# Kernel optimization log

Hardware: AMD Instinct MI355X
Metric: run time of the kernel (lower is better)

## Reference

```python
import jax, jax.numpy as jnp
import numpy as np

RANK = 4
ALPHA = 4.0
SCALE = ALPHA / RANK


def setup_inputs() -> dict:
    key = jax.random.key(0)
    k1, k2, k3, k4 = jax.random.split(key, 4)
    B, S, H = 4, 2048, 2048
    NH, HD = 16, 128
    x = jax.random.normal(k1, (B, S, H), dtype=jnp.float32)
    W_orig = jax.random.normal(k2, (H, NH, HD), dtype=jnp.float32) * (1.0 / np.sqrt(H))
    A_kernel = jax.random.normal(k3, (H, RANK), dtype=jnp.float32) * (1.0 / RANK)
    # B kernel is zero-init in the module; use small randn so the LoRA path is exercised
    B_kernel = jax.random.normal(k4, (RANK, NH, HD), dtype=jnp.float32) * 0.02
    return {"x": x, "W_orig": W_orig, "A_kernel": A_kernel, "B_kernel": B_kernel}


def reference(x, W_orig, A_kernel, B_kernel):
    # original layer: EinsumDense 'abc,cde->abde'  [B,S,H] x [H,NH,HD] -> [B,S,NH,HD]
    original_output = jnp.einsum('bsc,chd->bshd', x, W_orig)
    # LoRA path: Dense to rank, then EinsumDense back up, scaled
    ax = x @ A_kernel                                   # [B,S,r]
    lora_output = jnp.einsum('bsr,rhd->bshd', ax, B_kernel) * SCALE
    return original_output + lora_output
```

## Files before the change

### kernel.cpp

```cpp
#include <hip/hip_runtime.h>
#include <hip/hip_bf16.h>
#include <cstdint>


using bf16 = __hip_bfloat16;
typedef __attribute__((ext_vector_type(8))) __bf16 bf16x8;
typedef __attribute__((ext_vector_type(4))) float f32x4;

constexpr int Mdim = 8192;
constexpr int Ndim = 2048;
constexpr int Kdim = 2048;
constexpr float SCALE = 1.0f;

constexpr int BM = 256, BN = 256, BK = 64;
constexpr int NT2 = Kdim / (2 * BK);
constexpr int CVT_BLOCKS = (Mdim * Kdim) / (256 * 8);
constexpr int PREP_BLOCKS = (Ndim / 64) * (Kdim / 64);

__device__ __forceinline__ void gload_lds16(const void* g, void* l) {
  __builtin_amdgcn_global_load_lds(
      (const __attribute__((address_space(1))) uint32_t*)g,
      (__attribute__((address_space(3))) uint32_t*)l,
      16, 0, 0);
}

__global__ void prep_all(const float* __restrict__ X,
                         const float* __restrict__ W,
                         const float* __restrict__ A,
                         const float* __restrict__ Bk,
                         uint16_t* __restrict__ Xb,
                         uint16_t* __restrict__ Wt) {
  __shared__ float tile[64][65];

  if (blockIdx.x < CVT_BLOCKS) {
    const int i = blockIdx.x * blockDim.x + threadIdx.x;
    const float4* Xv = (const float4*)X;
    float4 a = Xv[i * 2 + 0];
    float4 b = Xv[i * 2 + 1];
    uint16_t o[8];
    o[0] = __bfloat16_as_ushort(__float2bfloat16(a.x));
    o[1] = __bfloat16_as_ushort(__float2bfloat16(a.y));
    o[2] = __bfloat16_as_ushort(__float2bfloat16(a.z));
    o[3] = __bfloat16_as_ushort(__float2bfloat16(a.w));
    o[4] = __bfloat16_as_ushort(__float2bfloat16(b.x));
    o[5] = __bfloat16_as_ushort(__float2bfloat16(b.y));
    o[6] = __bfloat16_as_ushort(__float2bfloat16(b.z));
    o[7] = __bfloat16_as_ushort(__float2bfloat16(b.w));
    *reinterpret_cast<uint4*>(Xb + (size_t)i * 8) = *reinterpret_cast<uint4*>(o);
  } else {
    const int pid = blockIdx.x - CVT_BLOCKS;
    const int tx = threadIdx.x & 63;
    const int ty = threadIdx.x >> 6;
    const int n0 = (pid & 31) * 64, k0 = (pid >> 5) * 64;

    const int n = n0 + tx;
    const float b0 = Bk[0 * Ndim + n];
    const float b1 = Bk[1 * Ndim + n];
    const float b2 = Bk[2 * Ndim + n];
    const float b3 = Bk[3 * Ndim + n];

    for (int i = ty; i < 64; i += 4) {
      const int k = k0 + i;
      float w = W[(size_t)k * Ndim + n];
      w += SCALE * (A[k * 4 + 0] * b0 + A[k * 4 + 1] * b1 +
                    A[k * 4 + 2] * b2 + A[k * 4 + 3] * b3);
      tile[tx][i] = w;
    }
    __syncthreads();
    for (int i = ty; i < 64; i += 4) {
      Wt[(size_t)(n0 + i) * Kdim + (k0 + tx)] =
          __bfloat16_as_ushort(__float2bfloat16(tile[i][tx]));
    }
  }
}

#define FENCE() asm volatile("" ::: "memory")
#define VMW(N)  asm volatile("s_waitcnt vmcnt(" #N ")" ::: "memory")
#define PMID()                                                                 \
  do {                                                                         \
    FENCE();                                                                   \
    __builtin_amdgcn_s_barrier();                                              \
    asm volatile("s_waitcnt lgkmcnt(0)" ::: "memory");                         \
  } while (0)
#define PEND()                                                                 \
  do {                                                                         \
    FENCE();                                                                   \
    __builtin_amdgcn_s_barrier();                                              \
    FENCE();                                                                   \
  } while (0)

__global__ __launch_bounds__(512, 2) void gemm_8ph(
    const uint16_t* __restrict__ X, const uint16_t* __restrict__ Wt,
    float* __restrict__ out) {
  __shared__ uint16_t lds[65536];

  const int t = threadIdx.x;
  const int wave = t >> 6, lane = t & 63;
  const int wm = wave >> 2, wn = wave & 3;
  const int l15 = lane & 15, kg = lane >> 4;
  const int sw = l15 & 7;

  const int lid = blockIdx.x;
  const int xcd = lid & 7, loc = lid >> 3;
  const int by = xcd * 4 + (loc & 3);
  const int bx = loc >> 2;
  const int m0 = by * BM, n0 = bx * BN;

  const uint16_t* Ag = X + (size_t)m0 * Kdim;
  const uint16_t* Bg = Wt + (size_t)n0 * Kdim;

  const int r8 = lane >> 3;
  const int gc = (lane & 7) ^ r8;
  const int slot0 = wave * 2, slot1 = slot0 + 1;
  const size_t go0 = (size_t)(slot0 * 8 + r8) * Kdim + gc * 8;
  const size_t go1 = (size_t)(slot1 * 8 + r8) * Kdim + gc * 8;

  int aE[2], bE[2];
#pragma unroll
  for (int s2 = 0; s2 < 2; ++s2) {
    const int p = (s2 * 4 + kg) ^ sw;
    aE[s2] = (wm * 64 + l15) * 64 + p * 8;
    bE[s2] = (wn * 32 + l15) * 64 + p * 8;
  }

#define STAGE_A(buf, h, kt)                                                    \
  do {                                                                         \
    gload_lds16(Ag + go0 + (size_t)(h) * 128 * Kdim + (kt),                    \
                &lds[(buf) * 32768 + (h) * 8192 + slot0 * 512]);               \
    gload_lds16(Ag + go1 + (size_t)(h) * 128 * Kdim + (kt),                    \
                &lds[(buf) * 32768 + (h) * 8192 + slot1 * 512]);               \
  } while (0)
#define STAGE_B(buf, h, kt)                                                    \
  do {                                                                         \
    gload_lds16(Bg + go0 + (size_t)(h) * 128 * Kdim + (kt),                    \
                &lds[(buf) * 32768 + 16384 + (h) * 8192 + slot0 * 512]);       \
    gload_lds16(Bg + go1 + (size_t)(h) * 128 * Kdim + (kt),                    \
                &lds[(buf) * 32768 + 16384 + (h) * 8192 + slot1 * 512]);       \
  } while (0)

  bf16x8 a[4][2], b[2][2];
  f32x4 acc[8][4] = {};

#define READ_A(QM, buf)                                                        \
  do {                                                                         \
    _Pragma("unroll") for (int ii = 0; ii < 4; ++ii)                           \
        _Pragma("unroll") for (int s2 = 0; s2 < 2; ++s2)                       \
            a[ii][s2] = *reinterpret_cast<const bf16x8*>(                      \
                &lds[(buf) * 32768 + (QM) * 8192 + ii * 1024 + aE[s2]]);       \
  } while (0)
#define READ_B(QN, buf)                                                        \
  do {                                                                         \
    _Pragma("unroll") for (int jj = 0; jj < 2; ++jj)                           \
        _Pragma("unroll") for (int s2 = 0; s2 < 2; ++s2)                       \
            b[jj][s2] = *reinterpret_cast<const bf16x8*>(                      \
                &lds[(buf) * 32768 + 16384 + (QN) * 8192 + jj * 1024 +         \
                     bE[s2]]);                                                 \
  } while (0)
#define MMA(QM, QN)                                                            \
  do {                                                                         \
    __builtin_amdgcn_s_setprio(1);                                             \
    _Pragma("unroll") for (int s2 = 0; s2 < 2; ++s2)                           \
        _Pragma("unroll") for (int ii = 0; ii < 4; ++ii)                       \
            _Pragma("unroll") for (int jj = 0; jj < 2; ++jj)                   \
                acc[(QM) * 4 + ii][(QN) * 2 + jj] =                            \
                    __builtin_amdgcn_mfma_f32_16x16x32_bf16(                   \
                        a[ii][s2], b[jj][s2],                                  \
                        acc[(QM) * 4 + ii][(QN) * 2 + jj], 0, 0, 0);           \
    __builtin_amdgcn_s_setprio(0);                                             \
  } while (0)

  STAGE_A(0, 0, 0); STAGE_B(0, 0, 0); STAGE_A(0, 1, 0); STAGE_B(0, 1, 0);
  FENCE();
  STAGE_A(1, 0, BK); STAGE_B(1, 0, BK); STAGE_A(1, 1, BK);
  FENCE();
  VMW(6);
  __builtin_amdgcn_s_barrier();
  FENCE();

#pragma unroll 1
  for (int j = 0; j < NT2; ++j) {
    const int kt1 = j * 128 + 64;
    const int kn0 = j * 128 + 128;
    const int kn1 = j * 128 + 192;
    const bool full = (j < NT2 - 1);

    STAGE_B(1, 1, kt1);
    VMW(8);
    READ_A(0, 0); READ_B(0, 0);
    PMID(); MMA(0, 0); PEND();

    if (full) STAGE_A(0, 0, kn0);
    READ_B(1, 0);
    PMID(); MMA(0, 1); PEND();

    READ_A(1, 0); READ_B(0, 0);
    PMID(); MMA(1, 0); PEND();

    if (full) { STAGE_B(0, 0, kn0); STAGE_A(0, 1, kn0); VMW(8); }
    else      { VMW(2); }
    READ_B(1, 0);
    PMID(); MMA(1, 1); PEND();

    if (full) { STAGE_B(0, 1, kn0); VMW(8); }
    else      { VMW(0); }
    READ_A(0, 1); READ_B(0, 1);
    PMID(); MMA(0, 0); PEND();

    if (full) STAGE_A(1, 0, kn1);
    READ_B(1, 1);
    PMID(); MMA(0, 1); PEND();

    READ_A(1, 1); READ_B(0, 1);
    PMID(); MMA(1, 0); PEND();

    if (full) { STAGE_B(1, 0, kn1); STAGE_A(1, 1, kn1); VMW(8); }
    READ_B(1, 1);
    PMID(); MMA(1, 1); PEND();
  }

#pragma unroll
  for (int i = 0; i < 8; ++i) {
    const int mb = m0 + (i >> 2) * 128 + wm * 64 + (i & 3) * 16 + kg * 4;
#pragma unroll
    for (int jn = 0; jn < 4; ++jn) {
      const int n = n0 + (jn >> 1) * 128 + wn * 32 + (jn & 1) * 16 + l15;
#pragma unroll
      for (int r = 0; r < 4; ++r) {
        out[(size_t)(mb + r) * Ndim + n] = acc[i][jn][r];
      }
    }
  }
#undef STAGE_A
#undef STAGE_B
#undef READ_A
#undef READ_B
#undef MMA
}

extern "C" void kernel_launch(void* const* d_in, const int* in_sizes, int n_in,
                              void* d_out, int out_size, void* d_ws, size_t ws_size,
                              hipStream_t stream) {
  const float* x  = (const float*)d_in[0];
  const float* W  = (const float*)d_in[1];
  const float* A  = (const float*)d_in[2];
  const float* Bk = (const float*)d_in[3];
  float* out = (float*)d_out;

  uint16_t* Xb = (uint16_t*)d_ws;
  uint16_t* Wt = (uint16_t*)((char*)d_ws + (size_t)Mdim * Kdim * 2);

  prep_all<<<CVT_BLOCKS + PREP_BLOCKS, 256, 0, stream>>>(x, W, A, Bk, Xb, Wt);

  gemm_8ph<<<(Mdim / BM) * (Ndim / BN), 512, 0, stream>>>(Xb, Wt, out);
}
```

Measured before the change: 197.2 us.

## Double-buffer B fragments in registers and reorder MMA phases to cut LDS reads

Keeps two B register fragments (b0, b1) so the phase order becomes (0,0),(0,1),(1,1),(1,0). This lets each B fragment be reused across two MMA phases, removing two of the four B re-reads from LDS per half-iteration. The global-to-LDS staging schedule and vmcnt waits are rearranged to match, and an early lgkmcnt(8) wait is added. The cost is more VGPR pressure at a 2-wave occupancy target, and the hand-tuned waitcnt counts could create hazards if they are wrong.

```diff
diff --git a/kernel.cpp b/kernel.cpp
--- a/kernel.cpp
+++ b/kernel.cpp
@@ -76,6 +76,7 @@
 
 #define FENCE() asm volatile("" ::: "memory")
 #define VMW(N)  asm volatile("s_waitcnt vmcnt(" #N ")" ::: "memory")
+#define LGKM8() asm volatile("s_waitcnt lgkmcnt(8)" ::: "memory")
 #define PMID()                                                                 \
   do {                                                                         \
     FENCE();                                                                   \
@@ -138,7 +139,7 @@
                 &lds[(buf) * 32768 + 16384 + (h) * 8192 + slot1 * 512]);       \
   } while (0)
 
-  bf16x8 a[4][2], b[2][2];
+  bf16x8 a[4][2], b0[2][2], b1[2][2];
   f32x4 acc[8][4] = {};
 
 #define READ_A(QM, buf)                                                        \
@@ -148,15 +149,15 @@
             a[ii][s2] = *reinterpret_cast<const bf16x8*>(                      \
                 &lds[(buf) * 32768 + (QM) * 8192 + ii * 1024 + aE[s2]]);       \
   } while (0)
-#define READ_B(QN, buf)                                                        \
+#define READ_B(QN, buf, dst)                                                   \
   do {                                                                         \
     _Pragma("unroll") for (int jj = 0; jj < 2; ++jj)                           \
         _Pragma("unroll") for (int s2 = 0; s2 < 2; ++s2)                       \
-            b[jj][s2] = *reinterpret_cast<const bf16x8*>(                      \
+            dst[jj][s2] = *reinterpret_cast<const bf16x8*>(                    \
                 &lds[(buf) * 32768 + 16384 + (QN) * 8192 + jj * 1024 +         \
                      bE[s2]]);                                                 \
   } while (0)
-#define MMA(QM, QN)                                                            \
+#define MMA(QM, QN, barr)                                                      \
   do {                                                                         \
     __builtin_amdgcn_s_setprio(1);                                             \
     _Pragma("unroll") for (int s2 = 0; s2 < 2; ++s2)                           \
@@ -164,58 +165,58 @@
             _Pragma("unroll") for (int jj = 0; jj < 2; ++jj)                   \
                 acc[(QM) * 4 + ii][(QN) * 2 + jj] =                            \
                     __builtin_amdgcn_mfma_f32_16x16x32_bf16(                   \
-                        a[ii][s2], b[jj][s2],                                  \
+                        a[ii][s2], barr[jj][s2],                               \
                         acc[(QM) * 4 + ii][(QN) * 2 + jj], 0, 0, 0);           \
     __builtin_amdgcn_s_setprio(0);                                             \
   } while (0)
 
-  STAGE_A(0, 0, 0); STAGE_B(0, 0, 0); STAGE_A(0, 1, 0); STAGE_B(0, 1, 0);
+  STAGE_B(0, 0, 0); STAGE_A(0, 0, 0); STAGE_B(0, 1, 0); STAGE_A(0, 1, 0);
   FENCE();
-  STAGE_A(1, 0, BK); STAGE_B(1, 0, BK); STAGE_A(1, 1, BK);
+  STAGE_B(1, 0, BK); STAGE_A(1, 0, BK); STAGE_B(1, 1, BK); STAGE_A(1, 1, BK);
   FENCE();
-  VMW(6);
+  VMW(8);
   __builtin_amdgcn_s_barrier();
   FENCE();
 
 #pragma unroll 1
   for (int j = 0; j < NT2; ++j) {
-    const int kt1 = j * 128 + 64;
     const int kn0 = j * 128 + 128;
     const int kn1 = j * 128 + 192;
     const bool full = (j < NT2 - 1);
 
-    STAGE_B(1, 1, kt1);
-    VMW(8);
-    READ_A(0, 0); READ_B(0, 0);
-    PMID(); MMA(0, 0); PEND();
-
+    READ_A(0, 0); READ_B(0, 0, b0);
+    LGKM8();
+    PMID(); MMA(0, 0, b0); PEND();
+
+    READ_B(1, 0, b1);
+    if (full) STAGE_B(0, 0, kn0);
+    PMID(); MMA(0, 1, b1); PEND();
+
+    READ_A(1, 0);
     if (full) STAGE_A(0, 0, kn0);
-    READ_B(1, 0);
-    PMID(); MMA(0, 1); PEND();
-
-    READ_A(1, 0); READ_B(0, 0);
-    PMID(); MMA(1, 0); PEND();
-
-    if (full) { STAGE_B(0, 0, kn0); STAGE_A(0, 1, kn0); VMW(8); }
-    else      { VMW(2); }
-    READ_B(1, 0);
-    PMID(); MMA(1, 1); PEND();
-
-    if (full) { STAGE_B(0, 1, kn0); VMW(8); }
-    else      { VMW(0); }
-    READ_A(0, 1); READ_B(0, 1);
-    PMID(); MMA(0, 0); PEND();
-
+    PMID(); MMA(1, 1, b1); PEND();
+
+    if (full) { STAGE_B(0, 1, kn0); VMW(6); }
+    else      { VMW(4); }
+    PMID(); MMA(1, 0, b0); PEND();
+
+    READ_A(0, 1); READ_B(0, 1, b0);
+    if (full) STAGE_A(0, 1, kn0);
+    else      VMW(2);
+    LGKM8();
+    PMID(); MMA(0, 0, b0); PEND();
+
+    READ_B(1, 1, b1);
+    if (full) STAGE_B(1, 0, kn1);
+    else      VMW(0);
+    PMID(); MMA(0, 1, b1); PEND();
+
+    READ_A(1, 1);
     if (full) STAGE_A(1, 0, kn1);
-    READ_B(1, 1);
-    PMID(); MMA(0, 1); PEND();
-
-    READ_A(1, 1); READ_B(0, 1);
-    PMID(); MMA(1, 0); PEND();
-
-    if (full) { STAGE_B(1, 0, kn1); STAGE_A(1, 1, kn1); VMW(8); }
-    READ_B(1, 1);
-    PMID(); MMA(1, 1); PEND();
+    PMID(); MMA(1, 1, b1); PEND();
+
+    if (full) { STAGE_B(1, 1, kn1); STAGE_A(1, 1, kn1); VMW(8); }
+    PMID(); MMA(1, 0, b0); PEND();
   }
 
 #pragma unroll
```

Result: no change. 194.3 us (-1.5%).
